# Optimization experiments

Hardware: AMD Instinct MI355X
Metric: run time of the kernel (lower is better)

Reference implementation:

```python
import jax, jax.numpy as jnp
import numpy as np

B, T, D, K = 8, 1024, 256, 100
G, V = 2, 320
TEMP = 0.1
DIV_W = 0.1
L2_W = 10.0
DIV_EPS = 1e-7
COS_EPS = 1e-8


def setup_inputs() -> dict:
    key = jax.random.key(0)
    k1, k2, k3, k4, k5 = jax.random.split(key, 5)
    return {
        "quantized_features": jax.random.normal(k1, (B, T, D), jnp.float32),
        "context_features": jax.random.normal(k2, (B, T, D), jnp.float32),
        "codebook_logits": jax.random.normal(k3, (B, T, G, V), jnp.float32),
        "neg_idx": jax.random.randint(k4, (B, T, K), 0, T, jnp.int32),
        "mask": jax.random.bernoulli(k5, 0.5, (B, T)),
    }


def _losses(quantized_features, context_features, codebook_logits, neg_idx, mask):
    Bq, Tq, Dq = quantized_features.shape
    # --- contrastive loss ---
    # gather negatives: [B, T, K, D]
    negatives = quantized_features[jnp.arange(Bq)[:, None, None], neg_idx]
    # targets = [positive, negatives]: [B, T, K+1, D]
    targets = jnp.concatenate([quantized_features[:, :, None, :], negatives], axis=2)
    pred = context_features[:, :, None, :]  # [B, T, 1, D]
    dot = jnp.sum(pred * targets, axis=-1)  # [B, T, K+1]
    pn = jnp.sqrt(jnp.sum(pred * pred, axis=-1))      # [B, T, 1]
    tn = jnp.sqrt(jnp.sum(targets * targets, axis=-1))  # [B, T, K+1]
    cos = dot / jnp.maximum(pn * tn, COS_EPS)
    # kill positive-as-negative collisions (column 0 is the true positive)
    pos_is_neg = neg_idx == jnp.arange(Tq)[None, :, None]  # [B, T, K]
    collision = jnp.concatenate(
        [jnp.zeros((Bq, Tq, 1), dtype=bool), pos_is_neg], axis=2)
    logits = jnp.where(collision, -jnp.inf, cos) / TEMP
    # cross-entropy with target class 0, reduction='sum', over masked positions only
    logp0 = jax.nn.log_softmax(logits, axis=-1)[..., 0]  # [B, T]
    loss_c = -jnp.sum(jnp.where(mask, logp0, 0.0))

    # --- diversity loss ---
    probs = jax.nn.softmax(codebook_logits.astype(jnp.float32), axis=-1)  # [B,T,G,V]
    avg = probs.reshape(Bq * Tq, G, V).mean(axis=0)  # [G, V]
    entropy = -jnp.sum(avg * jnp.log(avg + DIV_EPS), axis=-1)  # [G]
    perplexity = jnp.exp(entropy)
    loss_d = jnp.sum(V - perplexity)

    # --- l2 norm loss ---
    loss_l2 = jnp.mean(quantized_features.astype(jnp.float32) ** 2)

    loss = loss_c + DIV_W * loss_d + L2_W * loss_l2
    return loss


def reference(quantized_features, context_features, codebook_logits, neg_idx, mask):
    return _losses(quantized_features, context_features, codebook_logits, neg_idx, mask)
```

## Files before the change

kernel.cpp:

```cpp
#include <hip/hip_runtime.h>
#include <hip/hip_bf16.h>
#include <math.h>

#define B_ 8
#define T_ 1024
#define D_ 256
#define K_ 100
#define G_ 2
#define V_ 320
#define NT_ 101
#define TEMP_ 0.1f
#define DIV_W_ 0.1f
#define L2_W_ 10.0f
#define DIV_EPS_ 1e-7f
#define COS_EPS_ 1e-8f

#define WS_LOSSC 0
#define WS_AVG   2
#define WS_FLAG  643
#define WS_SSQ   644
#define WS_QNORM 1024
#define WS_CNORM 9216
#define WS_LOSSP 17408
#define WS_QBF16 25600
#define WS_BF16_BYTES ((size_t)(WS_QBF16 + (size_t)B_ * T_ * D_ / 2) * 4)

#define NORM_BLOCKS 256
#define CB_BLOCKS   256

__device__ inline unsigned short f2bf_rne(float f) {
    unsigned int u = __float_as_uint(f);
    u += 0x7FFFu + ((u >> 16) & 1u);
    return (unsigned short)(u >> 16);
}

template <bool PACK_BF16>
__global__ __launch_bounds__(256) void prep_kernel(
    const float* __restrict__ q, const float* __restrict__ c,
    const float* __restrict__ cb, const unsigned int* __restrict__ maskw,
    float* __restrict__ ws)
{
    __shared__ float sh[G_ * V_];
    __shared__ int sA, sB;
    const int tid = threadIdx.x;
    const int lane = tid & 63;
    const int wavein = tid >> 6;
    const int blk = blockIdx.x;

    if (blk < NORM_BLOCKS) {
        const int b = blk & 7;
        const int seg = blk >> 3;
        float ssq = 0.0f;
#pragma unroll 1
        for (int i = 0; i < 8; i++) {
            const int r = b * T_ + seg * 32 + wavein * 8 + i;
            const float4 v = ((const float4*)(q + (size_t)r * D_))[lane];
            float s = v.x * v.x + v.y * v.y + v.z * v.z + v.w * v.w;
            ssq += s;
            if (PACK_BF16) {
                ushort4 pk;
                pk.x = f2bf_rne(v.x); pk.y = f2bf_rne(v.y);
                pk.z = f2bf_rne(v.z); pk.w = f2bf_rne(v.w);
                ((ushort4*)((char*)ws + (size_t)WS_QBF16 * 4 +
                            (size_t)r * 512))[lane] = pk;
            }
            const float4 w = ((const float4*)(c + (size_t)r * D_))[lane];
            float s2 = w.x * w.x + w.y * w.y + w.z * w.z + w.w * w.w;
#pragma unroll
            for (int sft = 32; sft >= 1; sft >>= 1) {
                s  += __shfl_xor(s, sft);
                s2 += __shfl_xor(s2, sft);
            }
            if (lane == 0) {
                ws[WS_QNORM + r] = sqrtf(s);
                ws[WS_CNORM + r] = sqrtf(s2);
            }
        }
#pragma unroll
        for (int sft = 32; sft >= 1; sft >>= 1) ssq += __shfl_xor(ssq, sft);
        if (lane == 0) sh[wavein] = ssq;
        __syncthreads();
        if (tid == 0)
            ws[WS_SSQ + blk] = sh[0] + sh[1] + sh[2] + sh[3];

        if (blk == 0) {
            if (tid == 0) { sA = 0; sB = 0; }
            __syncthreads();
            int a = 0, bb = 0;
            for (int i = tid; i < (B_ * T_) / 4; i += 256) {
                const unsigned int w = maskw[i];
                a  |= (w > 1u) ? 1 : 0;
                bb |= (w != 0u && w != 0x3F800000u) ? 1 : 0;
            }
            if (a)  atomicOr(&sA, 1);
            if (bb) atomicOr(&sB, 1);
            __syncthreads();
            if (tid == 0)
                ((int*)ws)[WS_FLAG] = (!sA) ? 0 : ((!sB) ? 1 : 2);
        }
    } else {
        for (int i = tid; i < G_ * V_; i += 256) sh[i] = 0.0f;
        __syncthreads();
        const int cblk = blk - NORM_BLOCKS;
        const int base = cblk * 4 + wavein;
        float r0[5] = {0, 0, 0, 0, 0};
        float r1[5] = {0, 0, 0, 0, 0};
        const bool odd = (base & 1);
#pragma unroll 1
        for (int i = 0; i < 16; i++) {
            const int r = base + 1024 * i;
            const float* row = cb + (size_t)r * V_;
            float v[5];
#pragma unroll
            for (int j = 0; j < 5; j++)
                v[j] = __builtin_nontemporal_load(&row[lane + 64 * j]);
            float mx = fmaxf(fmaxf(fmaxf(v[0], v[1]), fmaxf(v[2], v[3])), v[4]);
#pragma unroll
            for (int s = 32; s >= 1; s >>= 1) mx = fmaxf(mx, __shfl_xor(mx, s));
            float e[5], sum = 0.0f;
#pragma unroll
            for (int j = 0; j < 5; j++) { e[j] = __expf(v[j] - mx); sum += e[j]; }
#pragma unroll
            for (int s = 32; s >= 1; s >>= 1) sum += __shfl_xor(sum, s);
            const float is = 1.0f / sum;
            if (odd) {
#pragma unroll
                for (int j = 0; j < 5; j++) r1[j] += e[j] * is;
            } else {
#pragma unroll
                for (int j = 0; j < 5; j++) r0[j] += e[j] * is;
            }
        }
#pragma unroll
        for (int j = 0; j < 5; j++) {
            atomicAdd(&sh[0 * V_ + lane + 64 * j], r0[j]);
            atomicAdd(&sh[1 * V_ + lane + 64 * j], r1[j]);
        }
        __syncthreads();
        for (int i = tid; i < G_ * V_; i += 256)
            atomicAdd(&ws[WS_AVG + i], sh[i]);
    }
}

template <bool USE_BF16>
__global__ __launch_bounds__(256) void contrastive_kernel(
    const float* __restrict__ quant,
    const float* __restrict__ ctx,
    const int* __restrict__ negidx,
    const void* __restrict__ maskp,
    float* __restrict__ ws)
{
    const int cblk = blockIdx.x;
    const int b = cblk & 7;
    const int t = cblk >> 3;
    const int bt = b * T_ + t;

    const int tid = threadIdx.x;
    const int flag = ((const int*)ws)[WS_FLAG];
    bool m;
    if (flag == 2)      m = ((const unsigned char*)maskp)[bt] != 0;
    else if (flag == 1) m = ((const float*)maskp)[bt] != 0.0f;
    else                m = ((const int*)maskp)[bt] != 0;
    if (!m) {
        if (tid == 0) ws[WS_LOSSP + cblk] = 0.0f;
        return;
    }

    __shared__ float s_pred[D_];
    __shared__ int   s_idx[NT_ + 3];
    __shared__ float s_tn[NT_ + 3];
    __shared__ float s_logit[NT_ + 3];

    if (tid < 64)
        ((float4*)s_pred)[tid] = ((const float4*)(ctx + (size_t)bt * D_))[tid];
    if (tid < K_)
        s_idx[tid + 1] = negidx[(size_t)bt * K_ + tid];
    if (tid == K_)
        s_idx[0] = t;
    __syncthreads();
    if (tid < NT_) {
        const int idx = s_idx[tid];
        const bool col = (tid > 0) && (idx == t);
        s_tn[tid] = col ? -1.0f : ws[WS_QNORM + b * T_ + idx];
    }
    __syncthreads();

    const float pn = ws[WS_CNORM + bt];
    const int g = tid >> 2;
    const int p = tid & 3;

#pragma unroll
    for (int pass = 0; pass < 2; ++pass) {
        const int k = g + 64 * pass;
        if (k < NT_) {
            const int idx = s_idx[k];
            float dot = 0.0f;
            if (USE_BF16) {
                const uint4* row = (const uint4*)((const char*)ws +
                    (size_t)WS_QBF16 * 4 + (size_t)(b * T_ + idx) * 512);
                uint4 u[8];
#pragma unroll
                for (int i = 0; i < 8; ++i) u[i] = row[i * 4 + p];
#pragma unroll
                for (int i = 0; i < 8; ++i) {
                    const int J0 = (p + 4 * i) * 4;
                    const unsigned int w0 = u[i].x, w1 = u[i].y,
                                       w2 = u[i].z, w3 = u[i].w;
                    const float2 q0 = ((const float2*)s_pred)[J0 + 0];
                    const float2 q1 = ((const float2*)s_pred)[J0 + 1];
                    const float2 q2 = ((const float2*)s_pred)[J0 + 2];
                    const float2 q3 = ((const float2*)s_pred)[J0 + 3];
                    dot += __uint_as_float(w0 << 16) * q0.x
                         + __uint_as_float(w0 & 0xFFFF0000u) * q0.y
                         + __uint_as_float(w1 << 16) * q1.x
                         + __uint_as_float(w1 & 0xFFFF0000u) * q1.y
                         + __uint_as_float(w2 << 16) * q2.x
                         + __uint_as_float(w2 & 0xFFFF0000u) * q2.y
                         + __uint_as_float(w3 << 16) * q3.x
                         + __uint_as_float(w3 & 0xFFFF0000u) * q3.y;
                }
            } else {
                const float4* row = (const float4*)(quant +
                    ((size_t)b * T_ + idx) * D_);
                float4 r[16];
#pragma unroll
                for (int i = 0; i < 16; ++i) r[i] = row[i * 4 + p];
#pragma unroll
                for (int i = 0; i < 16; ++i) {
                    const float4 q = ((const float4*)s_pred)[i * 4 + p];
                    dot += r[i].x * q.x + r[i].y * q.y
                         + r[i].z * q.z + r[i].w * q.w;
                }
            }
            dot += __shfl_xor(dot, 1);
            dot += __shfl_xor(dot, 2);
            if (p == 0) {
                const float tn = s_tn[k];
                s_logit[k] = (tn < 0.0f) ? -1e30f
                    : (dot / fmaxf(pn * tn, COS_EPS_)) * (1.0f / TEMP_);
            }
        }
    }
    __syncthreads();

    if (tid < 64) {
        const float l0 = s_logit[tid];
        const float l1 = (tid + 64 < NT_) ? s_logit[tid + 64] : -1e30f;
        float mx = fmaxf(l0, l1);
#pragma unroll
        for (int s = 32; s >= 1; s >>= 1) mx = fmaxf(mx, __shfl_xor(mx, s));
        float sum = __expf(l0 - mx) + __expf(l1 - mx);
#pragma unroll
        for (int s = 32; s >= 1; s >>= 1) sum += __shfl_xor(sum, s);
        if (tid == 0) {
            const float logp0 = s_logit[0] - (mx + __logf(sum));
            ws[WS_LOSSP + cblk] = -logp0;
        }
    }
}

__global__ __launch_bounds__(256) void finalize_kernel(
    const float* __restrict__ ws, float* __restrict__ out)
{
    __shared__ float sred[4];
    const int tid = threadIdx.x;
    const int lane = tid & 63;
    const int wavein = tid >> 6;

    float lc = 0.0f;
    for (int i = tid; i < B_ * T_; i += 256) lc += ws[WS_LOSSP + i];
#pragma unroll
    for (int s = 32; s >= 1; s >>= 1) lc += __shfl_xor(lc, s);
    if (lane == 0) sred[wavein] = lc;
    __syncthreads();

    if (tid < 64) {
        float ss = 0.0f;
#pragma unroll
        for (int i = 0; i < 4; i++) ss += ws[WS_SSQ + lane + 64 * i];
        const float* avg = ws + WS_AVG;
        float e0 = 0.0f, e1 = 0.0f;
        const float inv = 1.0f / (float)(B_ * T_);
#pragma unroll
        for (int i = 0; i < 5; i++) {
            const float a0 = avg[0 * V_ + lane + 64 * i] * inv;
            const float a1 = avg[1 * V_ + lane + 64 * i] * inv;
            e0 -= a0 * __logf(a0 + DIV_EPS_);
            e1 -= a1 * __logf(a1 + DIV_EPS_);
        }
#pragma unroll
        for (int s = 32; s >= 1; s >>= 1) {
            ss += __shfl_xor(ss, s);
            e0 += __shfl_xor(e0, s);
            e1 += __shfl_xor(e1, s);
        }
        if (tid == 0) {
            const float loss_c = sred[0] + sred[1] + sred[2] + sred[3];
            const float loss_d = ((float)V_ - __expf(e0)) + ((float)V_ - __expf(e1));
            const float loss_l2 = ss / (float)(B_ * T_ * D_);
            out[0] = loss_c + DIV_W_ * loss_d + L2_W_ * loss_l2;
        }
    }
}

extern "C" void kernel_launch(void* const* d_in, const int* in_sizes, int n_in,
                              void* d_out, int out_size, void* d_ws, size_t ws_size,
                              hipStream_t stream) {
    const float* quant = (const float*)d_in[0];
    const float* ctx   = (const float*)d_in[1];
    const float* cb    = (const float*)d_in[2];
    const int*   nidx  = (const int*)d_in[3];
    const void*  mask  = d_in[4];
    float* ws  = (float*)d_ws;
    float* out = (float*)d_out;

    const bool bf16 = (ws_size >= WS_BF16_BYTES);

    hipMemsetAsync(d_ws, 0, (WS_SSQ) * sizeof(float), stream);

    if (bf16) {
        prep_kernel<true><<<NORM_BLOCKS + CB_BLOCKS, 256, 0, stream>>>(
            quant, ctx, cb, (const unsigned int*)mask, ws);
        contrastive_kernel<true><<<B_ * T_, 256, 0, stream>>>(
            quant, ctx, nidx, mask, ws);
    } else {
        prep_kernel<false><<<NORM_BLOCKS + CB_BLOCKS, 256, 0, stream>>>(
            quant, ctx, cb, (const unsigned int*)mask, ws);
        contrastive_kernel<false><<<B_ * T_, 256, 0, stream>>>(
            quant, ctx, nidx, mask, ws);
    }
    finalize_kernel<<<1, 256, 0, stream>>>(ws, out);
}
```

Baseline: 134.6 us.

## Compute cosine norms inline in contrastive kernel instead of precomputing in prep

The prep kernel no longer reads the context features or writes per-row norm arrays. It now only packs quantized rows to bf16 and accumulates the squared sum, spread over twice as many smaller blocks. The contrastive kernel computes the prediction norm from the context row it already loads, and each target norm from the same gathered bf16 row used for the dot product. This removes a global gather, a barrier, and a full pass over the context tensor. In exchange it roughly doubles the FMA work per gathered row, and target norms are now taken from bf16-rounded values rather than fp32.

New measurement: 136.5 us. No clear change (+1.4%).

```diff
diff --git a/kernel.cpp b/kernel.cpp
--- a/kernel.cpp
+++ b/kernel.cpp
@@ -15,17 +15,15 @@
 #define DIV_EPS_ 1e-7f
 #define COS_EPS_ 1e-8f
 
-#define WS_LOSSC 0
 #define WS_AVG   2
 #define WS_FLAG  643
 #define WS_SSQ   644
-#define WS_QNORM 1024
-#define WS_CNORM 9216
+#define WS_ZERO_TOP WS_SSQ
 #define WS_LOSSP 17408
 #define WS_QBF16 25600
 #define WS_BF16_BYTES ((size_t)(WS_QBF16 + (size_t)B_ * T_ * D_ / 2) * 4)
 
-#define NORM_BLOCKS 256
+#define NORM_BLOCKS 512
 #define CB_BLOCKS   256
 
 __device__ inline unsigned short f2bf_rne(float f) {
@@ -36,9 +34,8 @@
 
 template <bool PACK_BF16>
 __global__ __launch_bounds__(256) void prep_kernel(
-    const float* __restrict__ q, const float* __restrict__ c,
-    const float* __restrict__ cb, const unsigned int* __restrict__ maskw,
-    float* __restrict__ ws)
+    const float* __restrict__ q, const float* __restrict__ cb,
+    const unsigned int* __restrict__ maskw, float* __restrict__ ws)
 {
     __shared__ float sh[G_ * V_];
     __shared__ int sA, sB;
@@ -51,29 +48,17 @@
         const int b = blk & 7;
         const int seg = blk >> 3;
         float ssq = 0.0f;
-#pragma unroll 1
-        for (int i = 0; i < 8; i++) {
-            const int r = b * T_ + seg * 32 + wavein * 8 + i;
+#pragma unroll
+        for (int i = 0; i < 4; i++) {
+            const int r = b * T_ + seg * 16 + wavein * 4 + i;
             const float4 v = ((const float4*)(q + (size_t)r * D_))[lane];
-            float s = v.x * v.x + v.y * v.y + v.z * v.z + v.w * v.w;
-            ssq += s;
+            ssq += v.x * v.x + v.y * v.y + v.z * v.z + v.w * v.w;
             if (PACK_BF16) {
                 ushort4 pk;
                 pk.x = f2bf_rne(v.x); pk.y = f2bf_rne(v.y);
                 pk.z = f2bf_rne(v.z); pk.w = f2bf_rne(v.w);
                 ((ushort4*)((char*)ws + (size_t)WS_QBF16 * 4 +
                             (size_t)r * 512))[lane] = pk;
-            }
-            const float4 w = ((const float4*)(c + (size_t)r * D_))[lane];
-            float s2 = w.x * w.x + w.y * w.y + w.z * w.z + w.w * w.w;
-#pragma unroll
-            for (int sft = 32; sft >= 1; sft >>= 1) {
-                s  += __shfl_xor(s, sft);
-                s2 += __shfl_xor(s2, sft);
-            }
-            if (lane == 0) {
-                ws[WS_QNORM + r] = sqrtf(s);
-                ws[WS_CNORM + r] = sqrtf(s2);
             }
         }
 #pragma unroll
@@ -167,25 +152,26 @@
     }
 
     __shared__ float s_pred[D_];
+    __shared__ float s_pn;
     __shared__ int   s_idx[NT_ + 3];
-    __shared__ float s_tn[NT_ + 3];
     __shared__ float s_logit[NT_ + 3];
 
-    if (tid < 64)
-        ((float4*)s_pred)[tid] = ((const float4*)(ctx + (size_t)bt * D_))[tid];
-    if (tid < K_)
-        s_idx[tid + 1] = negidx[(size_t)bt * K_ + tid];
-    if (tid == K_)
+    if (tid < 64) {
+        const float4 v = ((const float4*)(ctx + (size_t)bt * D_))[tid];
+        ((float4*)s_pred)[tid] = v;
+        float s = v.x * v.x + v.y * v.y + v.z * v.z + v.w * v.w;
+#pragma unroll
+        for (int sh = 32; sh >= 1; sh >>= 1) s += __shfl_xor(s, sh);
+        if (tid == 0) s_pn = sqrtf(s);
+    } else if (tid < 64 + K_) {
+        s_idx[tid - 63] =
+            __builtin_nontemporal_load(&negidx[(size_t)bt * K_ + (tid - 64)]);
+    } else if (tid == 64 + K_) {
         s_idx[0] = t;
+    }
     __syncthreads();
-    if (tid < NT_) {
-        const int idx = s_idx[tid];
-        const bool col = (tid > 0) && (idx == t);
-        s_tn[tid] = col ? -1.0f : ws[WS_QNORM + b * T_ + idx];
-    }
-    __syncthreads();
-
-    const float pn = ws[WS_CNORM + bt];
+
+    const float pn = s_pn;
     const int g = tid >> 2;
     const int p = tid & 3;
 
@@ -194,7 +180,7 @@
         const int k = g + 64 * pass;
         if (k < NT_) {
             const int idx = s_idx[k];
-            float dot = 0.0f;
+            float dot = 0.0f, tn2 = 0.0f;
             if (USE_BF16) {
                 const uint4* row = (const uint4*)((const char*)ws +
                     (size_t)WS_QBF16 * 4 + (size_t)(b * T_ + idx) * 512);
@@ -210,14 +196,18 @@
                     const float2 q1 = ((const float2*)s_pred)[J0 + 1];
                     const float2 q2 = ((const float2*)s_pred)[J0 + 2];
                     const float2 q3 = ((const float2*)s_pred)[J0 + 3];
-                    dot += __uint_as_float(w0 << 16) * q0.x
-                         + __uint_as_float(w0 & 0xFFFF0000u) * q0.y
-                         + __uint_as_float(w1 << 16) * q1.x
-                         + __uint_as_float(w1 & 0xFFFF0000u) * q1.y
-                         + __uint_as_float(w2 << 16) * q2.x
-                         + __uint_as_float(w2 & 0xFFFF0000u) * q2.y
-                         + __uint_as_float(w3 << 16) * q3.x
-                         + __uint_as_float(w3 & 0xFFFF0000u) * q3.y;
+                    const float a0 = __uint_as_float(w0 << 16);
+                    const float a1 = __uint_as_float(w0 & 0xFFFF0000u);
+                    const float a2 = __uint_as_float(w1 << 16);
+                    const float a3 = __uint_as_float(w1 & 0xFFFF0000u);
+                    const float a4 = __uint_as_float(w2 << 16);
+                    const float a5 = __uint_as_float(w2 & 0xFFFF0000u);
+                    const float a6 = __uint_as_float(w3 << 16);
+                    const float a7 = __uint_as_float(w3 & 0xFFFF0000u);
+                    dot += a0 * q0.x + a1 * q0.y + a2 * q1.x + a3 * q1.y
+                         + a4 * q2.x + a5 * q2.y + a6 * q3.x + a7 * q3.y;
+                    tn2 += a0 * a0 + a1 * a1 + a2 * a2 + a3 * a3
+                         + a4 * a4 + a5 * a5 + a6 * a6 + a7 * a7;
                 }
             } else {
                 const float4* row = (const float4*)(quant +
@@ -230,14 +220,17 @@
                     const float4 q = ((const float4*)s_pred)[i * 4 + p];
                     dot += r[i].x * q.x + r[i].y * q.y
                          + r[i].z * q.z + r[i].w * q.w;
+                    tn2 += r[i].x * r[i].x + r[i].y * r[i].y
+                         + r[i].z * r[i].z + r[i].w * r[i].w;
                 }
             }
             dot += __shfl_xor(dot, 1);
             dot += __shfl_xor(dot, 2);
+            tn2 += __shfl_xor(tn2, 1);
+            tn2 += __shfl_xor(tn2, 2);
             if (p == 0) {
-                const float tn = s_tn[k];
-                s_logit[k] = (tn < 0.0f) ? -1e30f
-                    : (dot / fmaxf(pn * tn, COS_EPS_)) * (1.0f / TEMP_);
+                s_logit[k] = (k > 0 && idx == t) ? -1e30f
+                    : (dot / fmaxf(pn * sqrtf(tn2), COS_EPS_)) * (1.0f / TEMP_);
             }
         }
     }
@@ -277,7 +270,7 @@
     if (tid < 64) {
         float ss = 0.0f;
 #pragma unroll
-        for (int i = 0; i < 4; i++) ss += ws[WS_SSQ + lane + 64 * i];
+        for (int i = 0; i < 8; i++) ss += ws[WS_SSQ + lane + 64 * i];
         const float* avg = ws + WS_AVG;
         float e0 = 0.0f, e1 = 0.0f;
         const float inv = 1.0f / (float)(B_ * T_);
@@ -316,16 +309,16 @@
 
     const bool bf16 = (ws_size >= WS_BF16_BYTES);
 
-    hipMemsetAsync(d_ws, 0, (WS_SSQ) * sizeof(float), stream);
+    hipMemsetAsync(d_ws, 0, (WS_ZERO_TOP) * sizeof(float), stream);
 
     if (bf16) {
         prep_kernel<true><<<NORM_BLOCKS + CB_BLOCKS, 256, 0, stream>>>(
-            quant, ctx, cb, (const unsigned int*)mask, ws);
+            quant, cb, (const unsigned int*)mask, ws);
         contrastive_kernel<true><<<B_ * T_, 256, 0, stream>>>(
             quant, ctx, nidx, mask, ws);
     } else {
         prep_kernel<false><<<NORM_BLOCKS + CB_BLOCKS, 256, 0, stream>>>(
-            quant, ctx, cb, (const unsigned int*)mask, ws);
+            quant, cb, (const unsigned int*)mask, ws);
         contrastive_kernel<false><<<B_ * T_, 256, 0, stream>>>(
             quant, ctx, nidx, mask, ws);
     }
```
